# Kernel tuning notes

Hardware: AMD Instinct MI355X
Metric: run time of the kernel (lower is better)

Reference implementation:

```python
import jax, jax.numpy as jnp
import numpy as np

B, T, D = 4096, 200, 64
NEG_INF = -(2.0 ** 32) + 1.0  # matches tf paddings constant


def setup_inputs() -> dict:
    key = jax.random.key(0)
    ks = jax.random.split(key, 12)
    queries = jax.random.normal(ks[0], (B, D), dtype=jnp.float32)
    keys = jax.random.normal(ks[1], (B, T, D), dtype=jnp.float32)
    keys_length = jax.random.randint(ks[2], (B,), 0, 200, dtype=jnp.int32)
    # attention MLP params (glorot-ish scale)
    W1 = jax.random.normal(ks[3], (4 * D, 16), dtype=jnp.float32) * (1.0 / np.sqrt(4 * D))
    b1 = jnp.zeros((16,), dtype=jnp.float32)
    W2 = jax.random.normal(ks[4], (16, 8), dtype=jnp.float32) * (1.0 / np.sqrt(16))
    b2 = jnp.zeros((8,), dtype=jnp.float32)
    W3 = jax.random.normal(ks[5], (8, 1), dtype=jnp.float32) * (1.0 / np.sqrt(8))
    b3 = jnp.zeros((1,), dtype=jnp.float32)
    W4 = jax.random.normal(ks[6], (D, D), dtype=jnp.float32) * (1.0 / np.sqrt(D))
    b4 = jnp.zeros((D,), dtype=jnp.float32)
    return {"queries": queries, "keys": keys, "keys_length": keys_length,
            "W1": W1, "b1": b1, "W2": W2, "b2": b2, "W3": W3, "b3": b3,
            "W4": W4, "b4": b4}


def reference(queries, keys, keys_length, W1, b1, W2, b2, W3, b3, W4, b4):
    Bq, Tq, Dq = keys.shape
    # tile queries across time: [B, T, D]
    q = jnp.broadcast_to(queries[:, None, :], (Bq, Tq, Dq))
    # DIN feature construction: [B, T, 4D]
    din_all = jnp.concatenate([q, keys, q - keys, q * keys], axis=-1)
    # tiny MLP scorer
    x = jax.nn.sigmoid(jnp.einsum('btf,fh->bth', din_all, W1) + b1)
    x = jax.nn.sigmoid(jnp.einsum('bth,hk->btk', x, W2) + b2)
    scores = (jnp.einsum('btk,ko->bto', x, W3) + b3)[..., 0]  # [B, T]
    # mask invalid history positions
    mask = jnp.arange(Tq, dtype=keys_length.dtype)[None, :] < keys_length[:, None]
    scores = jnp.where(mask, scores, NEG_INF)
    scores = scores / (Dq ** 0.5)  # scaling applied after masking, as in tf code
    attn = jax.nn.softmax(scores, axis=-1)  # [B, T]
    out = jnp.einsum('bt,btd->bd', attn, keys)  # weighted sum of keys
    out = out @ W4 + b4  # [B, D]
    return out
```

## Files before the change

### kernel.cpp

```cpp
#include <hip/hip_runtime.h>
#include <math.h>

#define TT 200
#define MTS 72

typedef __attribute__((ext_vector_type(8))) short bf16x8;
typedef __attribute__((ext_vector_type(4))) float f32x4;
typedef __attribute__((ext_vector_type(4))) float fv4;

union BF8 { bf16x8 v; unsigned u[4]; };

__device__ __forceinline__ float sigmoidf_(float x) {
    return 1.0f / (1.0f + __expf(-x));
}
__device__ __forceinline__ unsigned cvtpk(float a, float b) {
    unsigned r;
    asm("v_cvt_pk_bf16_f32 %0, %1, %2" : "=v"(r) : "v"(a), "v"(b));
    return r;
}
__device__ __forceinline__ short f2bf(float x) {
    unsigned u = __float_as_uint(x);
    u += 0x7fff + ((u >> 16) & 1);
    return (short)(u >> 16);
}
__device__ __forceinline__ float bf2f(short s) {
    return __uint_as_float(((unsigned)(unsigned short)s) << 16);
}
__device__ __forceinline__ float4 ldnt4(const float* p) {
    fv4 t = __builtin_nontemporal_load((const fv4*)p);
    float4 r;
    r.x = t[0]; r.y = t[1]; r.z = t[2]; r.w = t[3];
    return r;
}

__global__ __launch_bounds__(256, 4) void din_attn_flash(
    const float* __restrict__ queries,
    const float* __restrict__ keys,
    const int*   __restrict__ keys_length,
    const float* __restrict__ W1,
    const float* __restrict__ b1,
    const float* __restrict__ W2,
    const float* __restrict__ b2,
    const float* __restrict__ W3,
    const float* __restrict__ b3,
    const float* __restrict__ W4,
    const float* __restrict__ b4,
    float* __restrict__ out,
    int Bn)
{
    __shared__ __align__(16) short MtHi[4][16 * MTS];
    __shared__ __align__(16) short MtLo[4][16 * MTS];
    __shared__ __align__(16) float vS[4][64];

    const int tid  = threadIdx.x;
    const int w    = tid >> 6;
    const int lane = tid & 63;
    const int m16  = lane & 15;
    const int quad = lane >> 4;

    const int b = blockIdx.x * 4 + w;
    if (b >= Bn) return;
    const float* kb = keys + (size_t)b * (TT * 64);

    const float* kp0 = kb + m16 * 64 + quad * 8;
    float4 c0 = ldnt4(kp0);
    float4 c1 = ldnt4(kp0 + 4);
    float4 c2 = ldnt4(kp0 + 32);
    float4 c3 = ldnt4(kp0 + 36);
    const float* kp1 = kp0 + 16 * 64;
    float4 n0 = ldnt4(kp1);
    float4 n1 = ldnt4(kp1 + 4);
    float4 n2 = ldnt4(kp1 + 32);
    float4 n3 = ldnt4(kp1 + 36);

    const int len = __builtin_amdgcn_readfirstlane(keys_length[b]);

    float cp0 = 0.f, cp1 = 0.f, cp2 = 0.f, cp3 = 0.f;
    {
        const int d2 = lane >> 2;
        const int hg = lane & 3;
        const float4* W1v = (const float4*)W1;
        #pragma unroll
        for (int dg = 0; dg < 4; dg++) {
            const int d = dg * 16 + d2;
            const float q = queries[b * 64 + d];
            float4 a  = W1v[(0   + d) * 4 + hg];
            float4 bb = W1v[(64  + d) * 4 + hg];
            float4 cc = W1v[(128 + d) * 4 + hg];
            float4 dd = W1v[(192 + d) * 4 + hg];
            float mv0 = bb.x - cc.x + q * dd.x;
            float mv1 = bb.y - cc.y + q * dd.y;
            float mv2 = bb.z - cc.z + q * dd.z;
            float mv3 = bb.w - cc.w + q * dd.w;
            cp0 += q * (a.x + cc.x);
            cp1 += q * (a.y + cc.y);
            cp2 += q * (a.z + cc.z);
            cp3 += q * (a.w + cc.w);
            const int hb = hg * 4;
            short h0 = f2bf(mv0), h1 = f2bf(mv1), h2 = f2bf(mv2), h3 = f2bf(mv3);
            MtHi[w][(hb + 0) * MTS + d] = h0;
            MtHi[w][(hb + 1) * MTS + d] = h1;
            MtHi[w][(hb + 2) * MTS + d] = h2;
            MtHi[w][(hb + 3) * MTS + d] = h3;
            MtLo[w][(hb + 0) * MTS + d] = f2bf(mv0 - bf2f(h0));
            MtLo[w][(hb + 1) * MTS + d] = f2bf(mv1 - bf2f(h1));
            MtLo[w][(hb + 2) * MTS + d] = f2bf(mv2 - bf2f(h2));
            MtLo[w][(hb + 3) * MTS + d] = f2bf(mv3 - bf2f(h3));
        }
        #pragma unroll
        for (int mask = 4; mask <= 32; mask <<= 1) {
            cp0 += __shfl_xor(cp0, mask, 64);
            cp1 += __shfl_xor(cp1, mask, 64);
            cp2 += __shfl_xor(cp2, mask, 64);
            cp3 += __shfl_xor(cp3, mask, 64);
        }
    }
    float cv4[4];
    cv4[0] = __shfl(cp0, quad, 64) + b1[quad * 4 + 0];
    cv4[1] = __shfl(cp1, quad, 64) + b1[quad * 4 + 1];
    cv4[2] = __shfl(cp2, quad, 64) + b1[quad * 4 + 2];
    cv4[3] = __shfl(cp3, quad, 64) + b1[quad * 4 + 3];

    asm volatile("" ::: "memory");
    __builtin_amdgcn_wave_barrier();

    const int bb0 = m16 * MTS + quad * 8;
    const bf16x8 Bh0 = *(const bf16x8*)&MtHi[w][bb0];
    const bf16x8 Bh1 = *(const bf16x8*)&MtHi[w][bb0 + 32];
    const bf16x8 Bl0 = *(const bf16x8*)&MtLo[w][bb0];
    const bf16x8 Bl1 = *(const bf16x8*)&MtLo[w][bb0 + 32];

    BF8 a2;
    {
        float w2f[4];
        #pragma unroll
        for (int j = 0; j < 4; j++)
            w2f[j] = (m16 < 8) ? W2[(quad * 4 + j) * 8 + m16] : 0.0f;
        a2.u[0] = cvtpk(w2f[0], w2f[1]);
        a2.u[1] = cvtpk(w2f[2], w2f[3]);
        a2.u[2] = 0u;
        a2.u[3] = 0u;
    }

    const float4 b2a = *(const float4*)(b2);
    const float4 b2b = *(const float4*)(b2 + 4);
    const float4 w3a = *(const float4*)(W3);
    const float4 w3b = *(const float4*)(W3 + 4);
    const float  b3v = b3[0];
    const float b2k0 = quad == 0 ? b2a.x : (quad == 1 ? b2b.x : 0.f);
    const float b2k1 = quad == 0 ? b2a.y : (quad == 1 ? b2b.y : 0.f);
    const float b2k2 = quad == 0 ? b2a.z : (quad == 1 ? b2b.z : 0.f);
    const float b2k3 = quad == 0 ? b2a.w : (quad == 1 ? b2b.w : 0.f);
    const float w3k0 = quad == 0 ? w3a.x : (quad == 1 ? w3b.x : 0.f);
    const float w3k1 = quad == 0 ? w3a.y : (quad == 1 ? w3b.y : 0.f);
    const float w3k2 = quad == 0 ? w3a.z : (quad == 1 ? w3b.z : 0.f);
    const float w3k3 = quad == 0 ? w3a.w : (quad == 1 ? w3b.w : 0.f);

    const float M = 0.125f * (fabsf(b3v)
                  + fabsf(w3a.x) + fabsf(w3a.y) + fabsf(w3a.z) + fabsf(w3a.w)
                  + fabsf(w3b.x) + fabsf(w3b.y) + fabsf(w3b.z) + fabsf(w3b.w));

    const int lenEff = (len == 0) ? TT : len;
    const int ntiles = (lenEff + 15) >> 4;

    float ssum = 0.0f;
    float o[16];
    #pragma unroll
    for (int j = 0; j < 16; j++) o[j] = 0.0f;

    const float4 z4 = {0.f, 0.f, 0.f, 0.f};
    #define LOADT(TL, A0, A1, A2, A3)                                   \
        { const int t_ = (TL) * 16 + m16;                               \
          if (t_ < lenEff) {                                            \
              const float* p_ = kb + t_ * 64 + quad * 8;                \
              A0 = ldnt4(p_);                                           \
              A1 = ldnt4(p_ + 4);                                       \
              A2 = ldnt4(p_ + 32);                                      \
              A3 = ldnt4(p_ + 36);                                      \
          } else { A0 = z4; A1 = z4; A2 = z4; A3 = z4; } }

    for (int tile = 0; tile < ntiles; tile++) {
        float4 m0, m1, m2, m3;
        LOADT(tile + 2, m0, m1, m2, m3);

        BF8 ah0, ah1;
        ah0.u[0] = cvtpk(c0.x, c0.y);  ah0.u[1] = cvtpk(c0.z, c0.w);
        ah0.u[2] = cvtpk(c1.x, c1.y);  ah0.u[3] = cvtpk(c1.z, c1.w);
        ah1.u[0] = cvtpk(c2.x, c2.y);  ah1.u[1] = cvtpk(c2.z, c2.w);
        ah1.u[2] = cvtpk(c3.x, c3.y);  ah1.u[3] = cvtpk(c3.z, c3.w);

        f32x4 acc = {0.f, 0.f, 0.f, 0.f};
        acc = __builtin_amdgcn_mfma_f32_16x16x32_bf16(Bh0, ah0.v, acc, 0, 0, 0);
        acc = __builtin_amdgcn_mfma_f32_16x16x32_bf16(Bl0, ah0.v, acc, 0, 0, 0);
        acc = __builtin_amdgcn_mfma_f32_16x16x32_bf16(Bh1, ah1.v, acc, 0, 0, 0);
        acc = __builtin_amdgcn_mfma_f32_16x16x32_bf16(Bl1, ah1.v, acc, 0, 0, 0);

        const float h10 = sigmoidf_(acc[0] + cv4[0]);
        const float h11 = sigmoidf_(acc[1] + cv4[1]);
        const float h12 = sigmoidf_(acc[2] + cv4[2]);
        const float h13 = sigmoidf_(acc[3] + cv4[3]);
        BF8 hb;
        hb.u[0] = cvtpk(h10, h11);
        hb.u[1] = cvtpk(h12, h13);
        hb.u[2] = 0u;
        hb.u[3] = 0u;

        f32x4 acc2 = {0.f, 0.f, 0.f, 0.f};
        acc2 = __builtin_amdgcn_mfma_f32_16x16x32_bf16(a2.v, hb.v, acc2, 0, 0, 0);

        float s3p;
        s3p = sigmoidf_(acc2[0] + b2k0) * w3k0;
        s3p = fmaf(sigmoidf_(acc2[1] + b2k1), w3k1, s3p);
        s3p = fmaf(sigmoidf_(acc2[2] + b2k2), w3k2, s3p);
        s3p = fmaf(sigmoidf_(acc2[3] + b2k3), w3k3, s3p);
        s3p += __shfl_xor(s3p, 16, 64);
        s3p += __shfl_xor(s3p, 32, 64);

        const int tg = tile * 16 + m16;
        float sc = (len == 0) ? 0.0f : (s3p + b3v) * 0.125f;
        if (tg >= lenEff) sc = -1.0e30f;
        const float p = __expf(sc - M);

        ssum += p;
        o[0]  = fmaf(p, c0.x, o[0]);
        o[1]  = fmaf(p, c0.y, o[1]);
        o[2]  = fmaf(p, c0.z, o[2]);
        o[3]  = fmaf(p, c0.w, o[3]);
        o[4]  = fmaf(p, c1.x, o[4]);
        o[5]  = fmaf(p, c1.y, o[5]);
        o[6]  = fmaf(p, c1.z, o[6]);
        o[7]  = fmaf(p, c1.w, o[7]);
        o[8]  = fmaf(p, c2.x, o[8]);
        o[9]  = fmaf(p, c2.y, o[9]);
        o[10] = fmaf(p, c2.z, o[10]);
        o[11] = fmaf(p, c2.w, o[11]);
        o[12] = fmaf(p, c3.x, o[12]);
        o[13] = fmaf(p, c3.y, o[13]);
        o[14] = fmaf(p, c3.z, o[14]);
        o[15] = fmaf(p, c3.w, o[15]);

        c0 = n0; c1 = n1; c2 = n2; c3 = n3;
        n0 = m0; n1 = m1; n2 = m2; n3 = m3;
    }
    #undef LOADT

    #pragma unroll
    for (int mask = 1; mask <= 8; mask <<= 1) {
        ssum += __shfl_xor(ssum, mask, 64);
        #pragma unroll
        for (int j = 0; j < 16; j++) o[j] += __shfl_xor(o[j], mask, 64);
    }
    const float inv = 1.0f / ssum;
    if (m16 == 0) {
        #pragma unroll
        for (int j = 0; j < 8; j++) vS[w][quad * 8 + j]      = o[j] * inv;
        #pragma unroll
        for (int j = 0; j < 8; j++) vS[w][32 + quad * 8 + j] = o[8 + j] * inv;
    }
    asm volatile("" ::: "memory");
    __builtin_amdgcn_wave_barrier();

    float po = b4[lane];
    const float4* vS4 = (const float4*)&vS[w][0];
    #pragma unroll 4
    for (int d0 = 0; d0 < 16; d0++) {
        const float4 vv = vS4[d0];
        const float* w4p = W4 + d0 * 256 + lane;
        po = fmaf(vv.x, w4p[0],   po);
        po = fmaf(vv.y, w4p[64],  po);
        po = fmaf(vv.z, w4p[128], po);
        po = fmaf(vv.w, w4p[192], po);
    }
    out[(size_t)b * 64 + lane] = po;
}

extern "C" void kernel_launch(void* const* d_in, const int* in_sizes, int n_in,
                              void* d_out, int out_size, void* d_ws, size_t ws_size,
                              hipStream_t stream) {
    const float* queries     = (const float*)d_in[0];
    const float* keys        = (const float*)d_in[1];
    const int*   keys_length = (const int*)  d_in[2];
    const float* W1 = (const float*)d_in[3];
    const float* b1 = (const float*)d_in[4];
    const float* W2 = (const float*)d_in[5];
    const float* b2 = (const float*)d_in[6];
    const float* W3 = (const float*)d_in[7];
    const float* b3 = (const float*)d_in[8];
    const float* W4 = (const float*)d_in[9];
    const float* b4 = (const float*)d_in[10];
    float* out = (float*)d_out;

    const int Bn = in_sizes[2];
    const int blocks = (Bn + 3) >> 2;
    din_attn_flash<<<blocks, 256, 0, stream>>>(
        queries, keys, keys_length, W1, b1, W2, b2, W3, b3, W4, b4, out, Bn);
}
```

Baseline: 289.1 us.

## Load key tiles coalesced and transpose through swizzled LDS for MFMA fragments

Each lane now loads contiguous float4 chunks of a 16-row key tile, so a wave reads 1 KB contiguous segments instead of strided row pieces. It converts them to bf16 and writes them into a per-wave XOR-swizzled LDS tile, from which the MFMA A-fragments are read back. The weighted-sum accumulation is reorganized so each lane keeps a float4 of output dims, with probabilities broadcast by shuffle. This cuts register use from 16 to 4 accumulators and shrinks the final reduction. The cost is extra LDS traffic and shuffles per tile, plus a three-way register rotation unrolled by macro.

```diff
diff --git a/kernel.cpp b/kernel.cpp
--- a/kernel.cpp
+++ b/kernel.cpp
@@ -9,6 +9,7 @@
 typedef __attribute__((ext_vector_type(4))) float fv4;
 
 union BF8 { bf16x8 v; unsigned u[4]; };
+struct G { float4 v[4]; };
 
 __device__ __forceinline__ float sigmoidf_(float x) {
     return 1.0f / (1.0f + __expf(-x));
@@ -50,6 +51,7 @@
 {
     __shared__ __align__(16) short MtHi[4][16 * MTS];
     __shared__ __align__(16) short MtLo[4][16 * MTS];
+    __shared__ __align__(16) unsigned short Kt[4][16 * 64];
     __shared__ __align__(16) float vS[4][64];
 
     const int tid  = threadIdx.x;
@@ -61,17 +63,18 @@
     const int b = blockIdx.x * 4 + w;
     if (b >= Bn) return;
     const float* kb = keys + (size_t)b * (TT * 64);
-
-    const float* kp0 = kb + m16 * 64 + quad * 8;
-    float4 c0 = ldnt4(kp0);
-    float4 c1 = ldnt4(kp0 + 4);
-    float4 c2 = ldnt4(kp0 + 32);
-    float4 c3 = ldnt4(kp0 + 36);
-    const float* kp1 = kp0 + 16 * 64;
-    float4 n0 = ldnt4(kp1);
-    float4 n1 = ldnt4(kp1 + 4);
-    float4 n2 = ldnt4(kp1 + 32);
-    float4 n3 = ldnt4(kp1 + 36);
+    char* ktb = (char*)&Kt[w][0];
+
+    const float4 z4 = {0.f, 0.f, 0.f, 0.f};
+    G g0, g1, g2;
+
+    {
+        const float* tb = kb + lane * 4;
+        #pragma unroll
+        for (int j = 0; j < 4; j++) g0.v[j] = ldnt4(tb + j * 256);
+        #pragma unroll
+        for (int j = 0; j < 4; j++) g1.v[j] = ldnt4(tb + 1024 + j * 256);
+    }
 
     const int len = __builtin_amdgcn_readfirstlane(keys_length[b]);
 
@@ -164,98 +167,109 @@
     const int ntiles = (lenEff + 15) >> 4;
 
     float ssum = 0.0f;
-    float o[16];
-    #pragma unroll
-    for (int j = 0; j < 16; j++) o[j] = 0.0f;
-
-    const float4 z4 = {0.f, 0.f, 0.f, 0.f};
-    #define LOADT(TL, A0, A1, A2, A3)                                   \
-        { const int t_ = (TL) * 16 + m16;                               \
-          if (t_ < lenEff) {                                            \
-              const float* p_ = kb + t_ * 64 + quad * 8;                \
-              A0 = ldnt4(p_);                                           \
-              A1 = ldnt4(p_ + 4);                                       \
-              A2 = ldnt4(p_ + 32);                                      \
-              A3 = ldnt4(p_ + 36);                                      \
-          } else { A0 = z4; A1 = z4; A2 = z4; A3 = z4; } }
-
-    for (int tile = 0; tile < ntiles; tile++) {
-        float4 m0, m1, m2, m3;
-        LOADT(tile + 2, m0, m1, m2, m3);
-
-        BF8 ah0, ah1;
-        ah0.u[0] = cvtpk(c0.x, c0.y);  ah0.u[1] = cvtpk(c0.z, c0.w);
-        ah0.u[2] = cvtpk(c1.x, c1.y);  ah0.u[3] = cvtpk(c1.z, c1.w);
-        ah1.u[0] = cvtpk(c2.x, c2.y);  ah1.u[1] = cvtpk(c2.z, c2.w);
-        ah1.u[2] = cvtpk(c3.x, c3.y);  ah1.u[3] = cvtpk(c3.z, c3.w);
-
-        f32x4 acc = {0.f, 0.f, 0.f, 0.f};
-        acc = __builtin_amdgcn_mfma_f32_16x16x32_bf16(Bh0, ah0.v, acc, 0, 0, 0);
-        acc = __builtin_amdgcn_mfma_f32_16x16x32_bf16(Bl0, ah0.v, acc, 0, 0, 0);
-        acc = __builtin_amdgcn_mfma_f32_16x16x32_bf16(Bh1, ah1.v, acc, 0, 0, 0);
-        acc = __builtin_amdgcn_mfma_f32_16x16x32_bf16(Bl1, ah1.v, acc, 0, 0, 0);
-
-        const float h10 = sigmoidf_(acc[0] + cv4[0]);
-        const float h11 = sigmoidf_(acc[1] + cv4[1]);
-        const float h12 = sigmoidf_(acc[2] + cv4[2]);
-        const float h13 = sigmoidf_(acc[3] + cv4[3]);
-        BF8 hb;
-        hb.u[0] = cvtpk(h10, h11);
-        hb.u[1] = cvtpk(h12, h13);
-        hb.u[2] = 0u;
-        hb.u[3] = 0u;
-
-        f32x4 acc2 = {0.f, 0.f, 0.f, 0.f};
-        acc2 = __builtin_amdgcn_mfma_f32_16x16x32_bf16(a2.v, hb.v, acc2, 0, 0, 0);
-
-        float s3p;
-        s3p = sigmoidf_(acc2[0] + b2k0) * w3k0;
-        s3p = fmaf(sigmoidf_(acc2[1] + b2k1), w3k1, s3p);
-        s3p = fmaf(sigmoidf_(acc2[2] + b2k2), w3k2, s3p);
-        s3p = fmaf(sigmoidf_(acc2[3] + b2k3), w3k3, s3p);
-        s3p += __shfl_xor(s3p, 16, 64);
-        s3p += __shfl_xor(s3p, 32, 64);
-
-        const int tg = tile * 16 + m16;
-        float sc = (len == 0) ? 0.0f : (s3p + b3v) * 0.125f;
-        if (tg >= lenEff) sc = -1.0e30f;
-        const float p = __expf(sc - M);
-
-        ssum += p;
-        o[0]  = fmaf(p, c0.x, o[0]);
-        o[1]  = fmaf(p, c0.y, o[1]);
-        o[2]  = fmaf(p, c0.z, o[2]);
-        o[3]  = fmaf(p, c0.w, o[3]);
-        o[4]  = fmaf(p, c1.x, o[4]);
-        o[5]  = fmaf(p, c1.y, o[5]);
-        o[6]  = fmaf(p, c1.z, o[6]);
-        o[7]  = fmaf(p, c1.w, o[7]);
-        o[8]  = fmaf(p, c2.x, o[8]);
-        o[9]  = fmaf(p, c2.y, o[9]);
-        o[10] = fmaf(p, c2.z, o[10]);
-        o[11] = fmaf(p, c2.w, o[11]);
-        o[12] = fmaf(p, c3.x, o[12]);
-        o[13] = fmaf(p, c3.y, o[13]);
-        o[14] = fmaf(p, c3.z, o[14]);
-        o[15] = fmaf(p, c3.w, o[15]);
-
-        c0 = n0; c1 = n1; c2 = n2; c3 = n3;
-        n0 = m0; n1 = m1; n2 = m2; n3 = m3;
-    }
-    #undef LOADT
-
-    #pragma unroll
-    for (int mask = 1; mask <= 8; mask <<= 1) {
-        ssum += __shfl_xor(ssum, mask, 64);
-        #pragma unroll
-        for (int j = 0; j < 16; j++) o[j] += __shfl_xor(o[j], mask, 64);
-    }
+    float4 o4 = z4;
+
+    #define CVTW(SRC)                                                        \
+        { _Pragma("unroll")                                                  \
+          for (int j = 0; j < 4; j++) {                                      \
+              const int row_ = j * 4 + quad;                                 \
+              uint2 val_;                                                    \
+              val_.x = cvtpk(SRC.v[j].x, SRC.v[j].y);                        \
+              val_.y = cvtpk(SRC.v[j].z, SRC.v[j].w);                        \
+              *(uint2*)(ktb + row_ * 128 + ((m16 * 8) ^ ((row_ & 7) << 4)))  \
+                  = val_;                                                    \
+          } }
+
+    #define FRD()                                                            \
+        { asm volatile("" ::: "memory");                                     \
+          const int offr_ = m16 * 128 + ((quad * 16) ^ ((m16 & 7) << 4));    \
+          ah0 = *(const bf16x8*)(ktb + offr_);                               \
+          ah1 = *(const bf16x8*)(ktb + (offr_ ^ 64));                        \
+          asm volatile("" ::: "memory"); }
+
+    bf16x8 ah0, ah1;
+
+    CVTW(g0)
+    FRD()
+
+    #define BODY(IN, MID, FAR, TI)                                           \
+    {                                                                        \
+              \
+        { const int TL_ = (TI) + 2;                                          \
+          const float* tb_ = kb + TL_ * 1024 + lane * 4;                     \
+          _Pragma("unroll")                                                  \
+          for (int j = 0; j < 4; j++) {                                      \
+              const int row_ = TL_ * 16 + j * 4 + quad;                      \
+              FAR.v[j] = (row_ < lenEff) ? ldnt4(tb_ + j * 256) : z4;        \
+          } }                                                                \
+                      \
+        CVTW(MID)                                                            \
+                                   \
+        f32x4 acc = {0.f, 0.f, 0.f, 0.f};                                    \
+        acc = __builtin_amdgcn_mfma_f32_16x16x32_bf16(Bh0, ah0, acc, 0,0,0); \
+        acc = __builtin_amdgcn_mfma_f32_16x16x32_bf16(Bl0, ah0, acc, 0,0,0); \
+        acc = __builtin_amdgcn_mfma_f32_16x16x32_bf16(Bh1, ah1, acc, 0,0,0); \
+        acc = __builtin_amdgcn_mfma_f32_16x16x32_bf16(Bl1, ah1, acc, 0,0,0); \
+        const float h10 = sigmoidf_(acc[0] + cv4[0]);                        \
+        const float h11 = sigmoidf_(acc[1] + cv4[1]);                        \
+        const float h12 = sigmoidf_(acc[2] + cv4[2]);                        \
+        const float h13 = sigmoidf_(acc[3] + cv4[3]);                        \
+        BF8 hb;                                                              \
+        hb.u[0] = cvtpk(h10, h11);                                           \
+        hb.u[1] = cvtpk(h12, h13);                                           \
+        hb.u[2] = 0u;                                                        \
+        hb.u[3] = 0u;                                                        \
+        f32x4 acc2 = {0.f, 0.f, 0.f, 0.f};                                   \
+        acc2 = __builtin_amdgcn_mfma_f32_16x16x32_bf16(a2.v, hb.v, acc2, 0,0,0); \
+        float s3p;                                                           \
+        s3p = sigmoidf_(acc2[0] + b2k0) * w3k0;                              \
+        s3p = fmaf(sigmoidf_(acc2[1] + b2k1), w3k1, s3p);                    \
+        s3p = fmaf(sigmoidf_(acc2[2] + b2k2), w3k2, s3p);                    \
+        s3p = fmaf(sigmoidf_(acc2[3] + b2k3), w3k3, s3p);                    \
+        s3p += __shfl_xor(s3p, 16, 64);                                      \
+        s3p += __shfl_xor(s3p, 32, 64);                                      \
+        const int tg_ = (TI) * 16 + m16;                                     \
+        float sc = (len == 0) ? 0.0f : (s3p + b3v) * 0.125f;                 \
+        if (tg_ >= lenEff) sc = -1.0e30f;                                    \
+        const float p = __expf(sc - M);                                      \
+        ssum += p;                                                           \
+          \
+        _Pragma("unroll")                                                    \
+        for (int j = 0; j < 4; j++) {                                        \
+            const float pj = __shfl(p, j * 4 + quad, 64);                    \
+            o4.x = fmaf(pj, IN.v[j].x, o4.x);                                \
+            o4.y = fmaf(pj, IN.v[j].y, o4.y);                                \
+            o4.z = fmaf(pj, IN.v[j].z, o4.z);                                \
+            o4.w = fmaf(pj, IN.v[j].w, o4.w);                                \
+        }                                                                    \
+                                             \
+        FRD()                                                                \
+    }
+
+    int i = 0;
+    while (true) {
+        BODY(g0, g1, g2, i) if (++i >= ntiles) break;
+        BODY(g1, g2, g0, i) if (++i >= ntiles) break;
+        BODY(g2, g0, g1, i) if (++i >= ntiles) break;
+    }
+    #undef BODY
+    #undef CVTW
+    #undef FRD
+
+    ssum += __shfl_xor(ssum, 1, 64);
+    ssum += __shfl_xor(ssum, 2, 64);
+    ssum += __shfl_xor(ssum, 4, 64);
+    ssum += __shfl_xor(ssum, 8, 64);
+    o4.x += __shfl_xor(o4.x, 16, 64);  o4.x += __shfl_xor(o4.x, 32, 64);
+    o4.y += __shfl_xor(o4.y, 16, 64);  o4.y += __shfl_xor(o4.y, 32, 64);
+    o4.z += __shfl_xor(o4.z, 16, 64);  o4.z += __shfl_xor(o4.z, 32, 64);
+    o4.w += __shfl_xor(o4.w, 16, 64);  o4.w += __shfl_xor(o4.w, 32, 64);
+
     const float inv = 1.0f / ssum;
-    if (m16 == 0) {
-        #pragma unroll
-        for (int j = 0; j < 8; j++) vS[w][quad * 8 + j]      = o[j] * inv;
-        #pragma unroll
-        for (int j = 0; j < 8; j++) vS[w][32 + quad * 8 + j] = o[8 + j] * inv;
+    if (lane < 16) {
+        float4 t;
+        t.x = o4.x * inv; t.y = o4.y * inv; t.z = o4.z * inv; t.w = o4.w * inv;
+        *(float4*)&vS[w][lane * 4] = t;
     }
     asm volatile("" ::: "memory");
     __builtin_amdgcn_wave_barrier();
```

New measurement: 287.8 us. Within noise of the previous version (-0.4%).
